# Kernel tuning notes

Measured on AMD Instinct MI355X. Metric: run time of the kernel, lower is better.

## Reference

```python
import jax, jax.numpy as jnp
import numpy as np

N = 100000   # nodes
E = 1600000  # edges
B = 64       # graphs
IN_CH = 6
HID = 64
EPS_BN = 1e-5


def _sage_conv(x, src, dst, Wl, bl, Wr, n_nodes):
    # PyG SAGEConv (mean aggr): out = lin_l(mean_{j in N(i)} x_j) + lin_r(x_i)
    msg = x[src]  # [E, F] gather
    s = jax.ops.segment_sum(msg, dst, num_segments=n_nodes)
    cnt = jax.ops.segment_sum(jnp.ones((msg.shape[0], 1), x.dtype), dst, num_segments=n_nodes)
    agg = s / jnp.maximum(cnt, 1.0)  # isolated nodes -> 0 (PyG scatter-mean behavior)
    return agg @ Wl + bl + x @ Wr


def _bn_relu(h, g, b):
    # BatchNorm1d over node dim (training stats, biased var), then ReLU
    mu = jnp.mean(h, axis=0)
    var = jnp.mean((h - mu) ** 2, axis=0)
    return jax.nn.relu((h - mu) * jax.lax.rsqrt(var + EPS_BN) * g + b)


def setup_inputs() -> dict:
    key = jax.random.key(0)
    ks = jax.random.split(key, 20)
    def w(k, shape, fan_in):
        return jax.random.normal(k, shape, jnp.float32) * (1.0 / np.sqrt(fan_in))
    inp = {
        'x': jax.random.normal(ks[0], (N, IN_CH), jnp.float32),
        'edge_index': jax.random.randint(ks[1], (2, E), 0, N, jnp.int64),
        'batch': jnp.sort(jax.random.randint(ks[2], (N,), 0, B, jnp.int64)),
        'W1l': w(ks[3], (IN_CH, HID), IN_CH), 'b1': jnp.zeros((HID,), jnp.float32), 'W1r': w(ks[4], (IN_CH, HID), IN_CH),
        'W2l': w(ks[5], (HID, HID), HID), 'b2': jnp.zeros((HID,), jnp.float32), 'W2r': w(ks[6], (HID, HID), HID),
        'W3l': w(ks[7], (HID, HID), HID), 'b3': jnp.zeros((HID,), jnp.float32), 'W3r': w(ks[8], (HID, HID), HID),
        'g1': jnp.ones((HID,), jnp.float32), 'be1': jnp.zeros((HID,), jnp.float32),
        'g2': jnp.ones((HID,), jnp.float32), 'be2': jnp.zeros((HID,), jnp.float32),
        'g3': jnp.ones((HID,), jnp.float32), 'be3': jnp.zeros((HID,), jnp.float32),
        'phW1': w(ks[9], (HID, 32), HID), 'phb1': jnp.zeros((32,), jnp.float32),
        'phW2': w(ks[10], (32, 3), 32), 'phb2': jnp.zeros((3,), jnp.float32),
        'trW1': w(ks[11], (HID, 16), HID), 'trb1': jnp.zeros((16,), jnp.float32),
        'trW2': w(ks[12], (16, 1), 16), 'trb2': jnp.zeros((1,), jnp.float32),
    }
    return inp


def reference(x, edge_index, batch, W1l, b1, W1r, W2l, b2, W2r, W3l, b3, W3r,
              g1, be1, g2, be2, g3, be3, phW1, phb1, phW2, phb2, trW1, trb1, trW2, trb2):
    src, dst = edge_index[0], edge_index[1]
    n = x.shape[0]
    h = _bn_relu(_sage_conv(x, src, dst, W1l, b1, W1r, n), g1, be1)
    h = _bn_relu(_sage_conv(h, src, dst, W2l, b2, W2r, n), g2, be2)
    h = _bn_relu(_sage_conv(h, src, dst, W3l, b3, W3r, n), g3, be3)
    # persistence-weighted attention: softmax over ALL nodes (dim=0), as in the original
    pw = x[:, 4]
    pw = pw - jnp.min(pw)
    attn = jax.nn.softmax(pw + 1e-8, axis=0)  # [N]
    h_att = h * attn[:, None]
    # global mean pool per graph
    s = jax.ops.segment_sum(h_att, batch, num_segments=B)
    cnt = jax.ops.segment_sum(jnp.ones((n, 1), h.dtype), batch, num_segments=B)
    pool = s / jnp.maximum(cnt, 1.0)
    phase_logits = jax.nn.relu(pool @ phW1 + phb1) @ phW2 + phb2
    transition_prob = jax.nn.sigmoid(jax.nn.relu(pool @ trW1 + trb1) @ trW2 + trb2)
    return (phase_logits, transition_prob)
```

## Files before the change

kernel.cpp:

```cpp
#include <hip/hip_runtime.h>
#include <hip/hip_fp16.h>
#include <cstdint>
#include <cstddef>


#define EPB 8192
#define NBIN 512
#define EPS_BN 1e-5f

typedef _Float16 f16x8 __attribute__((ext_vector_type(8)));
typedef float    f32x4 __attribute__((ext_vector_type(4)));
typedef float    f32x2 __attribute__((ext_vector_type(2)));

__global__ __launch_bounds__(256) void bucket_hist(const int* __restrict__ dst,
                                                   int* __restrict__ blockBin,
                                                   int* __restrict__ binTotal, int E)
{
    __shared__ int hist[NBIN];
    int t = threadIdx.x;
    for (int i = t; i < NBIN; i += 256) hist[i] = 0;
    __syncthreads();
    int e0 = blockIdx.x * EPB;
#pragma unroll
    for (int k = 0; k < 32; k++) {
        int e = e0 + (k << 8) + t;
        if (e < E) atomicAdd(&hist[dst[e] >> 8], 1);
    }
    __syncthreads();
    for (int i = t; i < NBIN; i += 256) {
        int c = hist[i];
        blockBin[blockIdx.x * NBIN + i] = c;
        if (c) atomicAdd(&binTotal[i], c);
    }
}

__global__ __launch_bounds__(512) void bin_scan_totals(const int* __restrict__ binTotal,
                                                       int* __restrict__ binBase,
                                                       int* __restrict__ rowptrN)
{
    __shared__ int s[NBIN];
    int t = threadIdx.x;
    int tot = binTotal[t];
    s[t] = tot;
    __syncthreads();
    for (int off = 1; off < NBIN; off <<= 1) {
        int v = (t >= off) ? s[t - off] : 0;
        __syncthreads();
        s[t] += v;
        __syncthreads();
    }
    binBase[t] = s[t] - tot;
    if (t == NBIN - 1) { binBase[NBIN] = s[t]; *rowptrN = s[t]; }
}

__global__ __launch_bounds__(256) void blockbin_offs(int* __restrict__ blockBin,
                                                     const int* __restrict__ binBase,
                                                     int nBlk)
{
    int wv   = threadIdx.x >> 6;
    int lane = threadIdx.x & 63;
    int bin  = blockIdx.x * 4 + wv;
    int carry = binBase[bin];
    for (int c0 = 0; c0 < nBlk; c0 += 64) {
        int blk = c0 + lane;
        int cnt = (blk < nBlk) ? blockBin[blk * NBIN + bin] : 0;
        int v = cnt;
#pragma unroll
        for (int d = 1; d < 64; d <<= 1) {
            int u = __shfl_up(v, d, 64);
            if (lane >= d) v += u;
        }
        if (blk < nBlk) blockBin[blk * NBIN + bin] = carry + v - cnt;
        carry += __shfl(v, 63, 64);
    }
}

__global__ __launch_bounds__(256) void bucket_scatter(const int* __restrict__ src,
                                                      const int* __restrict__ dst,
                                                      const int* __restrict__ blockBin,
                                                      int* __restrict__ epck, int E)
{
    __shared__ int cur[NBIN];
    int t = threadIdx.x;
    for (int i = t; i < NBIN; i += 256) cur[i] = blockBin[blockIdx.x * NBIN + i];
    __syncthreads();
    int e0 = blockIdx.x * EPB;
#pragma unroll
    for (int k = 0; k < 32; k++) {
        int e = e0 + (k << 8) + t;
        if (e < E) {
            int d = dst[e];
            int pos = atomicAdd(&cur[d >> 8], 1);
            epck[pos] = src[e] | ((d & 255) << 24);
        }
    }
}

__global__ __launch_bounds__(256) void csr_local(const int* __restrict__ epck,
                                                 const int* __restrict__ binBase,
                                                 int* __restrict__ rowptr,
                                                 int* __restrict__ eidx, int N)
{
    __shared__ int cnt[256], s[256], cur[256];
    int t = threadIdx.x, bkt = blockIdx.x;
    int base = binBase[bkt], nE = binBase[bkt + 1] - base;
    cnt[t] = 0;
    __syncthreads();
    for (int j = t; j < nE; j += 256)
        atomicAdd(&cnt[(unsigned)epck[base + j] >> 24], 1);
    __syncthreads();
    s[t] = cnt[t];
    __syncthreads();
    for (int off = 1; off < 256; off <<= 1) {
        int v = (t >= off) ? s[t - off] : 0;
        __syncthreads();
        s[t] += v;
        __syncthreads();
    }
    int excl = s[t] - cnt[t];
    cur[t] = excl;
    int node = (bkt << 8) + t;
    if (node < N) rowptr[node] = base + excl;
    __syncthreads();
    for (int j = t; j < nE; j += 256) {
        int v = epck[base + j];
        int pos = atomicAdd(&cur[(unsigned)v >> 24], 1);
        eidx[base + pos] = v & 0xFFFFFF;
    }
}

__global__ __launch_bounds__(256) void w_prep(const float* __restrict__ Wl,
                                              const float* __restrict__ Wr,
                                              __half* __restrict__ wf)
{
    int i = blockIdx.x * 256 + threadIdx.x;
    if (i >= 8192) return;
    int j    = i & 7;
    int m    = (i >> 3) & 15;
    int quad = (i >> 7) & 3;
    int tt   = (i >> 9) & 3;
    int q    = i >> 11;
    int k    = (q & 1) * 32 + quad * 8 + j;
    int col  = tt * 16 + m;
    const float* W = (q < 2) ? Wl : Wr;
    wf[i] = __float2half_rn(W[k * 64 + col]);
}

__global__ __launch_bounds__(256) void sage1_fused(
    const int* __restrict__ rowptr, const int* __restrict__ eidx,
    const float* __restrict__ x,
    const float* __restrict__ Wl, const float* __restrict__ bias,
    const float* __restrict__ Wr, float* __restrict__ out, int n)
{
    __shared__ float4 sWl[6 * 16];
    __shared__ float4 sWr[6 * 16];
    for (int i = threadIdx.x; i < 6 * 16; i += 256) {
        sWl[i] = ((const float4*)Wl)[i];
        sWr[i] = ((const float4*)Wr)[i];
    }
    __syncthreads();

    int node = blockIdx.x * 256 + threadIdx.x;
    if (node >= n) return;

    int b = rowptr[node], e = rowptr[node + 1];
    float a[6] = {0.f, 0.f, 0.f, 0.f, 0.f, 0.f};
    for (int j = b; j < e; j++) {
        int s = eidx[j];
        const float2* r = (const float2*)(x + (size_t)s * 6);
        float2 r0 = r[0], r1 = r[1], r2 = r[2];
        a[0] += r0.x; a[1] += r0.y; a[2] += r1.x;
        a[3] += r1.y; a[4] += r2.x; a[5] += r2.y;
    }
    float invd = 1.0f / fmaxf((float)(e - b), 1.0f);

    const float2* xr2 = (const float2*)(x + (size_t)node * 6);
    float2 x0 = xr2[0], x1 = xr2[1], x2 = xr2[2];
    float hh[6] = {x0.x, x0.y, x1.x, x1.y, x2.x, x2.y};

    float4 acc[16];
#pragma unroll
    for (int cg = 0; cg < 16; cg++) acc[cg] = ((const float4*)bias)[cg];
#pragma unroll
    for (int k = 0; k < 6; k++) {
        float am = a[k] * invd;
        float hk = hh[k];
#pragma unroll
        for (int cg = 0; cg < 16; cg++) {
            float4 wl = sWl[k * 16 + cg];
            float4 wr = sWr[k * 16 + cg];
            acc[cg].x = fmaf(am, wl.x, fmaf(hk, wr.x, acc[cg].x));
            acc[cg].y = fmaf(am, wl.y, fmaf(hk, wr.y, acc[cg].y));
            acc[cg].z = fmaf(am, wl.z, fmaf(hk, wr.z, acc[cg].z));
            acc[cg].w = fmaf(am, wl.w, fmaf(hk, wr.w, acc[cg].w));
        }
    }
    float4* orow = (float4*)(out + (size_t)node * 64);
#pragma unroll
    for (int cg = 0; cg < 16; cg++) orow[cg] = acc[cg];
}

__global__ __launch_bounds__(256) void bn_stats(const float* __restrict__ h,
                                                float* __restrict__ stats, size_t total)
{
    __shared__ float ls[64], lss[64];
    if (threadIdx.x < 64) { ls[threadIdx.x] = 0.f; lss[threadIdx.x] = 0.f; }
    __syncthreads();
    float s = 0.f, ss = 0.f;
    size_t stride = (size_t)gridDim.x * 256;
    for (size_t i = (size_t)blockIdx.x * 256 + threadIdx.x; i < total; i += stride) {
        float v = h[i];
        s += v;
        ss = fmaf(v, v, ss);
    }
    int c = threadIdx.x & 63;
    atomicAdd(&ls[c], s);
    atomicAdd(&lss[c], ss);
    __syncthreads();
    if (threadIdx.x < 64) {
        unsafeAtomicAdd(&stats[threadIdx.x], ls[threadIdx.x]);
        unsafeAtomicAdd(&stats[64 + threadIdx.x], lss[threadIdx.x]);
    }
}

__global__ __launch_bounds__(128) void stats_reduce(const float* __restrict__ tmp,
                                                    float* __restrict__ stats)
{
    int t = threadIdx.x;
    float s = 0.f;
#pragma unroll 8
    for (int k = 0; k < 64; k++) s += tmp[k * 128 + t];
    stats[t] = s;
}

__global__ __launch_bounds__(256) void bn_dual(const float* __restrict__ h,
                                               const float* __restrict__ stats,
                                               const float* __restrict__ g,
                                               const float* __restrict__ be,
                                               __half* __restrict__ h16,
                                               unsigned* __restrict__ h8,
                                               float invN, size_t total)
{
    size_t i4 = (size_t)blockIdx.x * 256 + threadIdx.x;
    if (i4 * 4 >= total) return;
    int c0 = (int)((i4 * 4) & 63);
    float v[4];
    float4 hv = ((const float4*)h)[i4];
    float hh[4] = {hv.x, hv.y, hv.z, hv.w};
#pragma unroll
    for (int j = 0; j < 4; j++) {
        int c = c0 + j;
        float mu  = stats[c] * invN;
        float var = stats[64 + c] * invN - mu * mu;
        float sc  = g[c] / sqrtf(var + EPS_BN);
        float sh  = fmaf(-mu, sc, be[c]);
        v[j] = fmaxf(fmaf(hh[j], sc, sh), 0.f);
    }
    float2 o16;
    ((__half2*)&o16)[0] = __floats2half2_rn(v[0], v[1]);
    ((__half2*)&o16)[1] = __floats2half2_rn(v[2], v[3]);
    ((float2*)h16)[i4] = o16;
    int p = __builtin_amdgcn_cvt_pk_fp8_f32(v[0], v[1], 0, false);
    p     = __builtin_amdgcn_cvt_pk_fp8_f32(v[2], v[3], p, true);
    h8[i4] = (unsigned)p;
}

__global__ __launch_bounds__(256) void aggpull8(const int* __restrict__ rowptr,
                                                const int* __restrict__ eidx,
                                                const unsigned* __restrict__ h8,
                                                __half* __restrict__ agg16, int n)
{
    int wid  = (blockIdx.x * 256 + threadIdx.x) >> 6;
    int lane = threadIdx.x & 63;
    int grp  = lane >> 4;
    int cq   = lane & 15;
    int node = wid * 4 + grp;
    if (node >= n) return;
    int b = rowptr[node], e = rowptr[node + 1];

    float4 a0 = {0,0,0,0}, a1 = {0,0,0,0}, a2 = {0,0,0,0}, a3 = {0,0,0,0};

#define EDGE(S, ACC)                                                            \
    {                                                                           \
        unsigned r_ = h8[(size_t)(S) * 16 + cq];                                \
        f32x2 lo_ = __builtin_amdgcn_cvt_pk_f32_fp8(r_, false);                 \
        f32x2 hi_ = __builtin_amdgcn_cvt_pk_f32_fp8(r_, true);                  \
        ACC.x += lo_[0]; ACC.y += lo_[1]; ACC.z += hi_[0]; ACC.w += hi_[1];     \
    }

    int j = b;
    for (; j + 4 <= e; j += 4) {
        int s0 = eidx[j], s1 = eidx[j + 1], s2 = eidx[j + 2], s3 = eidx[j + 3];
        EDGE(s0, a0) EDGE(s1, a1) EDGE(s2, a2) EDGE(s3, a3)
    }
    for (; j < e; j++) {
        int s = eidx[j];
        EDGE(s, a0)
    }
#undef EDGE

    float ax = a0.x + a1.x + a2.x + a3.x;
    float ay = a0.y + a1.y + a2.y + a3.y;
    float az = a0.z + a1.z + a2.z + a3.z;
    float aw = a0.w + a1.w + a2.w + a3.w;
    float invd = 1.0f / fmaxf((float)(e - b), 1.0f);
    __half2 o01 = __floats2half2_rn(ax * invd, ay * invd);
    __half2 o23 = __floats2half2_rn(az * invd, aw * invd);
    float2 ov;
    ((__half2*)&ov)[0] = o01;
    ((__half2*)&ov)[1] = o23;
    ((float2*)(agg16 + (size_t)node * 64))[cq] = ov;
}

__global__ __launch_bounds__(256) void mm_mfma(
    const __half* __restrict__ agg16, const __half* __restrict__ h16,
    const __half* __restrict__ wfh, const float* __restrict__ bias,
    float* __restrict__ out, float* __restrict__ statsTmp, int n)
{
    __shared__ float ls[64], lss[64];
    int t = threadIdx.x;
    if (t < 64) { ls[t] = 0.f; lss[t] = 0.f; }
    __syncthreads();

    int wv = t >> 6, lane = t & 63;
    int m = lane & 15, quad = lane >> 4;
    int node0 = (blockIdx.x * 4 + wv) * 16;

    if (node0 < n) {
        const f16x8* wf = (const f16x8*)wfh;

        int nodeA = node0 + m;
        if (nodeA >= n) nodeA = n - 1;

        const _Float16* arow = (const _Float16*)(agg16 + (size_t)nodeA * 64);
        const _Float16* hrow = (const _Float16*)(h16   + (size_t)nodeA * 64);
        f16x8 af[4];
        af[0] = *(const f16x8*)(arow + quad * 8);
        af[1] = *(const f16x8*)(arow + 32 + quad * 8);
        af[2] = *(const f16x8*)(hrow + quad * 8);
        af[3] = *(const f16x8*)(hrow + 32 + quad * 8);

#pragma unroll
        for (int tt = 0; tt < 4; tt++) {
            float bv = bias[tt * 16 + m];
            f32x4 c = {bv, bv, bv, bv};
#pragma unroll
            for (int q = 0; q < 4; q++)
                c = __builtin_amdgcn_mfma_f32_16x16x32_f16(
                        af[q], wf[((q * 4 + tt) * 4 + quad) * 16 + m], c, 0, 0, 0);
            float s = 0.f, ss = 0.f;
#pragma unroll
            for (int r = 0; r < 4; r++) {
                int row = node0 + quad * 4 + r;
                float v = (row < n) ? c[r] : 0.f;
                if (row < n) out[(size_t)row * 64 + tt * 16 + m] = v;
                s += v;
                ss = fmaf(v, v, ss);
            }
            s  += __shfl_xor(s, 16, 64);  s  += __shfl_xor(s, 32, 64);
            ss += __shfl_xor(ss, 16, 64); ss += __shfl_xor(ss, 32, 64);
            if (quad == 0) {
                atomicAdd(&ls[tt * 16 + m], s);
                atomicAdd(&lss[tt * 16 + m], ss);
            }
        }
    }
    __syncthreads();
    if (t < 64) {
        float* slot = statsTmp + (size_t)(blockIdx.x & 63) * 128;
        unsafeAtomicAdd(&slot[t], ls[t]);
        unsafeAtomicAdd(&slot[64 + t], lss[t]);
    }
}

__global__ __launch_bounds__(256) void bn_pool(
    const float* __restrict__ h, const float* __restrict__ stats,
    const float* __restrict__ g, const float* __restrict__ be,
    const float* __restrict__ x, const int* __restrict__ batch,
    float* __restrict__ rawpool, float invN, int N, int chunk)
{
    int wid  = blockIdx.x * 4 + (threadIdx.x >> 6);
    int lane = threadIdx.x & 63;
    int i0 = wid * chunk;
    if (i0 >= N) return;
    int i1 = min(i0 + chunk, N);

    float mu  = stats[lane] * invN;
    float var = stats[64 + lane] * invN - mu * mu;
    float sc  = g[lane] / sqrtf(var + EPS_BN);
    float sh  = fmaf(-mu, sc, be[lane]);

    int   cur = batch[i0];
    float acc = 0.f;
    for (int i = i0; i < i1; i++) {
        int bi = batch[i];
        if (bi != cur) {
            unsafeAtomicAdd(&rawpool[cur * 64 + lane], acc);
            acc = 0.f;
            cur = bi;
        }
        float w = expf(x[(size_t)i * 6 + 4]);
        float v = fmaxf(fmaf(h[(size_t)i * 64 + lane], sc, sh), 0.f);
        acc = fmaf(v, w, acc);
    }
    unsafeAtomicAdd(&rawpool[cur * 64 + lane], acc);
}

__global__ __launch_bounds__(256) void softmax_sum(const float* __restrict__ x,
                                                   float* __restrict__ sumexp, int n)
{
    float s = 0.f;
    int stride = gridDim.x * 256;
    for (int i = blockIdx.x * 256 + threadIdx.x; i < n; i += stride)
        s += expf(x[(size_t)i * 6 + 4]);
#pragma unroll
    for (int o = 32; o > 0; o >>= 1) s += __shfl_down(s, o, 64);
    __shared__ float wsum[4];
    if ((threadIdx.x & 63) == 0) wsum[threadIdx.x >> 6] = s;
    __syncthreads();
    if (threadIdx.x == 0)
        unsafeAtomicAdd(sumexp, wsum[0] + wsum[1] + wsum[2] + wsum[3]);
}

__global__ void seg_bounds(const int* __restrict__ batch, int* __restrict__ lb, int n)
{
    int b = threadIdx.x;
    if (b > 64) return;
    int lo = 0, hi = n;
    while (lo < hi) {
        int mid = (lo + hi) >> 1;
        if (batch[mid] < b) lo = mid + 1; else hi = mid;
    }
    lb[b] = lo;
}

__global__ __launch_bounds__(64) void heads_kernel(
    const float* __restrict__ rawpool, const float* __restrict__ sumexp,
    const int* __restrict__ lb,
    const float* __restrict__ phW1, const float* __restrict__ phb1,
    const float* __restrict__ phW2, const float* __restrict__ phb2,
    const float* __restrict__ trW1, const float* __restrict__ trb1,
    const float* __restrict__ trW2, const float* __restrict__ trb2,
    float* __restrict__ out)
{
    int b = blockIdx.x, t = threadIdx.x;
    __shared__ float p[64], h1[32], h2[16];
    float cnt = (float)(lb[b + 1] - lb[b]);
    p[t] = rawpool[b * 64 + t] / (sumexp[0] * fmaxf(cnt, 1.0f));
    __syncthreads();
    if (t < 32) {
        float s = phb1[t];
        for (int k = 0; k < 64; k++) s = fmaf(p[k], phW1[k * 32 + t], s);
        h1[t] = fmaxf(s, 0.f);
    } else if (t < 48) {
        int tt = t - 32;
        float s = trb1[tt];
        for (int k = 0; k < 64; k++) s = fmaf(p[k], trW1[k * 16 + tt], s);
        h2[tt] = fmaxf(s, 0.f);
    }
    __syncthreads();
    if (t < 3) {
        float s = phb2[t];
        for (int k = 0; k < 32; k++) s = fmaf(h1[k], phW2[k * 3 + t], s);
        out[b * 3 + t] = s;
    } else if (t == 63) {
        float s = trb2[0];
        for (int k = 0; k < 16; k++) s = fmaf(h2[k], trW2[k], s);
        out[192 + b] = 1.0f / (1.0f + expf(-s));
    }
}

extern "C" void kernel_launch(void* const* d_in, const int* in_sizes, int n_in,
                              void* d_out, int out_size, void* d_ws, size_t ws_size,
                              hipStream_t stream)
{
    const float* x     = (const float*)d_in[0];
    const int*   ei    = (const int*)d_in[1];
    const int*   batch = (const int*)d_in[2];
    const float* W1l = (const float*)d_in[3];
    const float* b1  = (const float*)d_in[4];
    const float* W1r = (const float*)d_in[5];
    const float* W2l = (const float*)d_in[6];
    const float* b2  = (const float*)d_in[7];
    const float* W2r = (const float*)d_in[8];
    const float* W3l = (const float*)d_in[9];
    const float* b3  = (const float*)d_in[10];
    const float* W3r = (const float*)d_in[11];
    const float* g1  = (const float*)d_in[12];
    const float* be1 = (const float*)d_in[13];
    const float* g2  = (const float*)d_in[14];
    const float* be2 = (const float*)d_in[15];
    const float* g3  = (const float*)d_in[16];
    const float* be3 = (const float*)d_in[17];
    const float* phW1 = (const float*)d_in[18];
    const float* phb1 = (const float*)d_in[19];
    const float* phW2 = (const float*)d_in[20];
    const float* phb2 = (const float*)d_in[21];
    const float* trW1 = (const float*)d_in[22];
    const float* trb1 = (const float*)d_in[23];
    const float* trW2 = (const float*)d_in[24];
    const float* trb2 = (const float*)d_in[25];

    const int N = in_sizes[0] / 6;
    const int E = in_sizes[1] / 2;
    const int* src = ei;
    const int* dst = ei + E;

    const int NB    = (N + 255) >> 8;
    const int nBlkA = (E + EPB - 1) / EPB;

    float* ws = (float*)d_ws;
    const size_t N64 = (size_t)N * 64;
    float*  hA      = ws;
    float*  hB      = ws + N64;
    __half* agg16   = (__half*)(ws + 2 * N64);
    __half* h16     = (__half*)(ws + 2 * N64 + N64 / 2);
    int*   epck     = (int*)(ws + 3 * N64);
    int*   eidx     = epck + E;
    int*   blockBin = eidx + E;
    int*   binTotal = blockBin + (size_t)nBlkA * NBIN;
    float* stats    = (float*)(binTotal + NBIN);
    float* statsTmp = stats + 384;
    float* rawpool  = statsTmp + 16384;
    float* sumexp   = rawpool + 4096;
    int*   binBase  = (int*)(sumexp + 4);
    int*   rowptr   = binBase + NBIN + 1;
    int*   lb       = rowptr + N + 1;
    __half* wfrag2  = (__half*)(lb + 72);
    __half* wfrag3  = wfrag2 + 8192;
    unsigned* h8    = (unsigned*)(wfrag3 + 8192);
    float* out      = (float*)d_out;

    const int nodeBlocks = (N + 255) / 256;
    const int aggBlocks  = (N + 15) / 16;
    const int mfmaBlocks = (N + 63) / 64;
    const int cvt4Blocks = (int)((N64 / 4 + 255) / 256);
    const int PBLK = 1024;
    const int chunk = (N + PBLK * 4 - 1) / (PBLK * 4);
    const float invN = 1.0f / (float)N;

    size_t zbytes = (char*)(sumexp + 4) - (char*)binTotal;
    hipMemsetAsync(binTotal, 0, zbytes, stream);
    softmax_sum<<<256, 256, 0, stream>>>(x, sumexp, N);
    seg_bounds<<<1, 128, 0, stream>>>(batch, lb, N);
    w_prep<<<32, 256, 0, stream>>>(W2l, W2r, wfrag2);
    w_prep<<<32, 256, 0, stream>>>(W3l, W3r, wfrag3);

    bucket_hist<<<nBlkA, 256, 0, stream>>>(dst, blockBin, binTotal, E);
    bin_scan_totals<<<1, NBIN, 0, stream>>>(binTotal, binBase, rowptr + N);
    blockbin_offs<<<NBIN / 4, 256, 0, stream>>>(blockBin, binBase, nBlkA);
    bucket_scatter<<<nBlkA, 256, 0, stream>>>(src, dst, blockBin, epck, E);
    csr_local<<<NB, 256, 0, stream>>>(epck, binBase, rowptr, eidx, N);

    sage1_fused<<<nodeBlocks, 256, 0, stream>>>(rowptr, eidx, x, W1l, b1, W1r, hA, N);
    bn_stats<<<1024, 256, 0, stream>>>(hA, stats, N64);
    bn_dual<<<cvt4Blocks, 256, 0, stream>>>(hA, stats, g1, be1, h16, h8, invN, N64);

    aggpull8<<<aggBlocks, 256, 0, stream>>>(rowptr, eidx, h8, agg16, N);
    mm_mfma<<<mfmaBlocks, 256, 0, stream>>>(agg16, h16, wfrag2, b2, hB,
                                            statsTmp, N);
    stats_reduce<<<1, 128, 0, stream>>>(statsTmp, stats + 128);
    bn_dual<<<cvt4Blocks, 256, 0, stream>>>(hB, stats + 128, g2, be2, h16, h8,
                                            invN, N64);

    aggpull8<<<aggBlocks, 256, 0, stream>>>(rowptr, eidx, h8, agg16, N);
    mm_mfma<<<mfmaBlocks, 256, 0, stream>>>(agg16, h16, wfrag3, b3, hA,
                                            statsTmp + 8192, N);
    stats_reduce<<<1, 128, 0, stream>>>(statsTmp + 8192, stats + 256);

    bn_pool<<<PBLK, 256, 0, stream>>>(hA, stats + 256, g3, be3, x, batch,
                                      rawpool, invN, N, chunk);
    heads_kernel<<<64, 64, 0, stream>>>(rawpool, sumexp, lb,
                                        phW1, phb1, phW2, phb2,
                                        trW1, trb1, trW2, trb2, out);
}
```

Measured before the change: 381.0 us.

## Fuse CSR local build with first SAGE layer aggregation and transform

```diff
diff --git a/kernel.cpp b/kernel.cpp
--- a/kernel.cpp
+++ b/kernel.cpp
@@ -96,37 +96,83 @@
     }
 }
 
-__global__ __launch_bounds__(256) void csr_local(const int* __restrict__ epck,
-                                                 const int* __restrict__ binBase,
-                                                 int* __restrict__ rowptr,
-                                                 int* __restrict__ eidx, int N)
-{
-    __shared__ int cnt[256], s[256], cur[256];
+__global__ __launch_bounds__(256) void csr_sage1(
+    const int* __restrict__ epck, const int* __restrict__ binBase,
+    const float* __restrict__ x,
+    const float* __restrict__ Wl, const float* __restrict__ bias,
+    const float* __restrict__ Wr,
+    int* __restrict__ rowptr, int* __restrict__ eidx,
+    float* __restrict__ out, int N)
+{
+    __shared__ int    cnt[256], scn[256], cur[256];
+    __shared__ float  a6[256 * 6];
+    __shared__ float4 sWl[96], sWr[96];
     int t = threadIdx.x, bkt = blockIdx.x;
     int base = binBase[bkt], nE = binBase[bkt + 1] - base;
     cnt[t] = 0;
+    if (t < 96) { sWl[t] = ((const float4*)Wl)[t]; sWr[t] = ((const float4*)Wr)[t]; }
+    for (int i = t; i < 1536; i += 256) a6[i] = 0.f;
     __syncthreads();
     for (int j = t; j < nE; j += 256)
         atomicAdd(&cnt[(unsigned)epck[base + j] >> 24], 1);
     __syncthreads();
-    s[t] = cnt[t];
+    scn[t] = cnt[t];
     __syncthreads();
     for (int off = 1; off < 256; off <<= 1) {
-        int v = (t >= off) ? s[t - off] : 0;
+        int v = (t >= off) ? scn[t - off] : 0;
         __syncthreads();
-        s[t] += v;
+        scn[t] += v;
         __syncthreads();
     }
-    int excl = s[t] - cnt[t];
+    int excl = scn[t] - cnt[t];
     cur[t] = excl;
     int node = (bkt << 8) + t;
     if (node < N) rowptr[node] = base + excl;
     __syncthreads();
     for (int j = t; j < nE; j += 256) {
-        int v = epck[base + j];
-        int pos = atomicAdd(&cur[(unsigned)v >> 24], 1);
-        eidx[base + pos] = v & 0xFFFFFF;
-    }
+        int v  = epck[base + j];
+        int dl = (unsigned)v >> 24;
+        int s_ = v & 0xFFFFFF;
+        int pos = atomicAdd(&cur[dl], 1);
+        eidx[base + pos] = s_;
+        const float2* r = (const float2*)(x + (size_t)s_ * 6);
+        float2 r0 = r[0], r1 = r[1], r2 = r[2];
+        atomicAdd(&a6[dl * 6 + 0], r0.x); atomicAdd(&a6[dl * 6 + 1], r0.y);
+        atomicAdd(&a6[dl * 6 + 2], r1.x); atomicAdd(&a6[dl * 6 + 3], r1.y);
+        atomicAdd(&a6[dl * 6 + 4], r2.x); atomicAdd(&a6[dl * 6 + 5], r2.y);
+    }
+    __syncthreads();
+    if (node >= N) return;
+
+    float invd = 1.0f / fmaxf((float)cnt[t], 1.0f);
+    float a[6];
+#pragma unroll
+    for (int k = 0; k < 6; k++) a[k] = a6[t * 6 + k] * invd;
+
+    const float2* xr2 = (const float2*)(x + (size_t)node * 6);
+    float2 x0 = xr2[0], x1 = xr2[1], x2 = xr2[2];
+    float hh[6] = {x0.x, x0.y, x1.x, x1.y, x2.x, x2.y};
+
+    float4 acc[16];
+#pragma unroll
+    for (int cg = 0; cg < 16; cg++) acc[cg] = ((const float4*)bias)[cg];
+#pragma unroll
+    for (int k = 0; k < 6; k++) {
+        float am = a[k];
+        float hk = hh[k];
+#pragma unroll
+        for (int cg = 0; cg < 16; cg++) {
+            float4 wl = sWl[k * 16 + cg];
+            float4 wr = sWr[k * 16 + cg];
+            acc[cg].x = fmaf(am, wl.x, fmaf(hk, wr.x, acc[cg].x));
+            acc[cg].y = fmaf(am, wl.y, fmaf(hk, wr.y, acc[cg].y));
+            acc[cg].z = fmaf(am, wl.z, fmaf(hk, wr.z, acc[cg].z));
+            acc[cg].w = fmaf(am, wl.w, fmaf(hk, wr.w, acc[cg].w));
+        }
+    }
+    float4* orow = (float4*)(out + (size_t)node * 64);
+#pragma unroll
+    for (int cg = 0; cg < 16; cg++) orow[cg] = acc[cg];
 }
 
 __global__ __launch_bounds__(256) void w_prep(const float* __restrict__ Wl,
@@ -144,60 +190,6 @@
     int col  = tt * 16 + m;
     const float* W = (q < 2) ? Wl : Wr;
     wf[i] = __float2half_rn(W[k * 64 + col]);
-}
-
-__global__ __launch_bounds__(256) void sage1_fused(
-    const int* __restrict__ rowptr, const int* __restrict__ eidx,
-    const float* __restrict__ x,
-    const float* __restrict__ Wl, const float* __restrict__ bias,
-    const float* __restrict__ Wr, float* __restrict__ out, int n)
-{
-    __shared__ float4 sWl[6 * 16];
-    __shared__ float4 sWr[6 * 16];
-    for (int i = threadIdx.x; i < 6 * 16; i += 256) {
-        sWl[i] = ((const float4*)Wl)[i];
-        sWr[i] = ((const float4*)Wr)[i];
-    }
-    __syncthreads();
-
-    int node = blockIdx.x * 256 + threadIdx.x;
-    if (node >= n) return;
-
-    int b = rowptr[node], e = rowptr[node + 1];
-    float a[6] = {0.f, 0.f, 0.f, 0.f, 0.f, 0.f};
-    for (int j = b; j < e; j++) {
-        int s = eidx[j];
-        const float2* r = (const float2*)(x + (size_t)s * 6);
-        float2 r0 = r[0], r1 = r[1], r2 = r[2];
-        a[0] += r0.x; a[1] += r0.y; a[2] += r1.x;
-        a[3] += r1.y; a[4] += r2.x; a[5] += r2.y;
-    }
-    float invd = 1.0f / fmaxf((float)(e - b), 1.0f);
-
-    const float2* xr2 = (const float2*)(x + (size_t)node * 6);
-    float2 x0 = xr2[0], x1 = xr2[1], x2 = xr2[2];
-    float hh[6] = {x0.x, x0.y, x1.x, x1.y, x2.x, x2.y};
-
-    float4 acc[16];
-#pragma unroll
-    for (int cg = 0; cg < 16; cg++) acc[cg] = ((const float4*)bias)[cg];
-#pragma unroll
-    for (int k = 0; k < 6; k++) {
-        float am = a[k] * invd;
-        float hk = hh[k];
-#pragma unroll
-        for (int cg = 0; cg < 16; cg++) {
-            float4 wl = sWl[k * 16 + cg];
-            float4 wr = sWr[k * 16 + cg];
-            acc[cg].x = fmaf(am, wl.x, fmaf(hk, wr.x, acc[cg].x));
-            acc[cg].y = fmaf(am, wl.y, fmaf(hk, wr.y, acc[cg].y));
-            acc[cg].z = fmaf(am, wl.z, fmaf(hk, wr.z, acc[cg].z));
-            acc[cg].w = fmaf(am, wl.w, fmaf(hk, wr.w, acc[cg].w));
-        }
-    }
-    float4* orow = (float4*)(out + (size_t)node * 64);
-#pragma unroll
-    for (int cg = 0; cg < 16; cg++) orow[cg] = acc[cg];
 }
 
 __global__ __launch_bounds__(256) void bn_stats(const float* __restrict__ h,
@@ -531,7 +523,6 @@
     unsigned* h8    = (unsigned*)(wfrag3 + 8192);
     float* out      = (float*)d_out;
 
-    const int nodeBlocks = (N + 255) / 256;
     const int aggBlocks  = (N + 15) / 16;
     const int mfmaBlocks = (N + 63) / 64;
     const int cvt4Blocks = (int)((N64 / 4 + 255) / 256);
@@ -550,9 +541,9 @@
     bin_scan_totals<<<1, NBIN, 0, stream>>>(binTotal, binBase, rowptr + N);
     blockbin_offs<<<NBIN / 4, 256, 0, stream>>>(blockBin, binBase, nBlkA);
     bucket_scatter<<<nBlkA, 256, 0, stream>>>(src, dst, blockBin, epck, E);
-    csr_local<<<NB, 256, 0, stream>>>(epck, binBase, rowptr, eidx, N);
-
-    sage1_fused<<<nodeBlocks, 256, 0, stream>>>(rowptr, eidx, x, W1l, b1, W1r, hA, N);
+    csr_sage1<<<NB, 256, 0, stream>>>(epck, binBase, x, W1l, b1, W1r,
+                                      rowptr, eidx, hA, N);
+
     bn_stats<<<1024, 256, 0, stream>>>(hA, stats, N64);
     bn_dual<<<cvt4Blocks, 256, 0, stream>>>(hA, stats, g1, be1, h16, h8, invN, N64);
 
```

New measurement: 419.6 us. 10.1% more time.

## Fuse neighbor aggregation into MFMA matmul kernel via shared-memory tile

Applied to the files above, without the earlier changes.

```diff
diff --git a/kernel.cpp b/kernel.cpp
--- a/kernel.cpp
+++ b/kernel.cpp
@@ -265,78 +265,71 @@
     h8[i4] = (unsigned)p;
 }
 
-__global__ __launch_bounds__(256) void aggpull8(const int* __restrict__ rowptr,
-                                                const int* __restrict__ eidx,
-                                                const unsigned* __restrict__ h8,
-                                                __half* __restrict__ agg16, int n)
-{
-    int wid  = (blockIdx.x * 256 + threadIdx.x) >> 6;
-    int lane = threadIdx.x & 63;
-    int grp  = lane >> 4;
-    int cq   = lane & 15;
-    int node = wid * 4 + grp;
-    if (node >= n) return;
-    int b = rowptr[node], e = rowptr[node + 1];
-
-    float4 a0 = {0,0,0,0}, a1 = {0,0,0,0}, a2 = {0,0,0,0}, a3 = {0,0,0,0};
-
-#define EDGE(S, ACC)                                                            \
-    {                                                                           \
-        unsigned r_ = h8[(size_t)(S) * 16 + cq];                                \
-        f32x2 lo_ = __builtin_amdgcn_cvt_pk_f32_fp8(r_, false);                 \
-        f32x2 hi_ = __builtin_amdgcn_cvt_pk_f32_fp8(r_, true);                  \
-        ACC.x += lo_[0]; ACC.y += lo_[1]; ACC.z += hi_[0]; ACC.w += hi_[1];     \
-    }
-
-    int j = b;
-    for (; j + 4 <= e; j += 4) {
-        int s0 = eidx[j], s1 = eidx[j + 1], s2 = eidx[j + 2], s3 = eidx[j + 3];
-        EDGE(s0, a0) EDGE(s1, a1) EDGE(s2, a2) EDGE(s3, a3)
-    }
-    for (; j < e; j++) {
-        int s = eidx[j];
-        EDGE(s, a0)
-    }
-#undef EDGE
-
-    float ax = a0.x + a1.x + a2.x + a3.x;
-    float ay = a0.y + a1.y + a2.y + a3.y;
-    float az = a0.z + a1.z + a2.z + a3.z;
-    float aw = a0.w + a1.w + a2.w + a3.w;
-    float invd = 1.0f / fmaxf((float)(e - b), 1.0f);
-    __half2 o01 = __floats2half2_rn(ax * invd, ay * invd);
-    __half2 o23 = __floats2half2_rn(az * invd, aw * invd);
-    float2 ov;
-    ((__half2*)&ov)[0] = o01;
-    ((__half2*)&ov)[1] = o23;
-    ((float2*)(agg16 + (size_t)node * 64))[cq] = ov;
-}
-
-__global__ __launch_bounds__(256) void mm_mfma(
-    const __half* __restrict__ agg16, const __half* __restrict__ h16,
+#define TSTRIDE 72
+__global__ __launch_bounds__(256) void agg_mm_mfma(
+    const int* __restrict__ rowptr, const int* __restrict__ eidx,
+    const unsigned* __restrict__ h8, const __half* __restrict__ h16,
     const __half* __restrict__ wfh, const float* __restrict__ bias,
     float* __restrict__ out, float* __restrict__ statsTmp, int n)
 {
     __shared__ float ls[64], lss[64];
+    __shared__ _Float16 sT[4][16 * TSTRIDE];
     int t = threadIdx.x;
     if (t < 64) { ls[t] = 0.f; lss[t] = 0.f; }
-    __syncthreads();
 
     int wv = t >> 6, lane = t & 63;
+    int node0 = (blockIdx.x * 4 + wv) * 16;
+
+    int grp = lane >> 4, cq = lane & 15;
+#pragma unroll 1
+    for (int r = 0; r < 4; r++) {
+        int node = node0 + r * 4 + grp;
+        int b = 0, e = 0;
+        if (node < n) { b = rowptr[node]; e = rowptr[node + 1]; }
+
+        float4 a0 = {0,0,0,0}, a1 = {0,0,0,0}, a2 = {0,0,0,0}, a3 = {0,0,0,0};
+#define EDGE(S, ACC)                                                            \
+        {                                                                       \
+            unsigned r_ = h8[(size_t)(S) * 16 + cq];                            \
+            f32x2 lo_ = __builtin_amdgcn_cvt_pk_f32_fp8(r_, false);             \
+            f32x2 hi_ = __builtin_amdgcn_cvt_pk_f32_fp8(r_, true);              \
+            ACC.x += lo_[0]; ACC.y += lo_[1]; ACC.z += hi_[0]; ACC.w += hi_[1]; \
+        }
+        int j = b;
+        for (; j + 4 <= e; j += 4) {
+            int s0 = eidx[j], s1 = eidx[j + 1], s2 = eidx[j + 2], s3 = eidx[j + 3];
+            EDGE(s0, a0) EDGE(s1, a1) EDGE(s2, a2) EDGE(s3, a3)
+        }
+        for (; j < e; j++) {
+            int s = eidx[j];
+            EDGE(s, a0)
+        }
+#undef EDGE
+        float ax = a0.x + a1.x + a2.x + a3.x;
+        float ay = a0.y + a1.y + a2.y + a3.y;
+        float az = a0.z + a1.z + a2.z + a3.z;
+        float aw = a0.w + a1.w + a2.w + a3.w;
+        float invd = 1.0f / fmaxf((float)(e - b), 1.0f);
+        __half2 o01 = __floats2half2_rn(ax * invd, ay * invd);
+        __half2 o23 = __floats2half2_rn(az * invd, aw * invd);
+        float2 ov;
+        ((__half2*)&ov)[0] = o01;
+        ((__half2*)&ov)[1] = o23;
+        *(float2*)(&sT[wv][(r * 4 + grp) * TSTRIDE + cq * 4]) = ov;
+    }
+    __syncthreads();
+
     int m = lane & 15, quad = lane >> 4;
-    int node0 = (blockIdx.x * 4 + wv) * 16;
-
     if (node0 < n) {
         const f16x8* wf = (const f16x8*)wfh;
 
         int nodeA = node0 + m;
         if (nodeA >= n) nodeA = n - 1;
 
-        const _Float16* arow = (const _Float16*)(agg16 + (size_t)nodeA * 64);
-        const _Float16* hrow = (const _Float16*)(h16   + (size_t)nodeA * 64);
+        const _Float16* hrow = (const _Float16*)(h16 + (size_t)nodeA * 64);
         f16x8 af[4];
-        af[0] = *(const f16x8*)(arow + quad * 8);
-        af[1] = *(const f16x8*)(arow + 32 + quad * 8);
+        af[0] = *(const f16x8*)(&sT[wv][m * TSTRIDE + quad * 8]);
+        af[1] = *(const f16x8*)(&sT[wv][m * TSTRIDE + 32 + quad * 8]);
         af[2] = *(const f16x8*)(hrow + quad * 8);
         af[3] = *(const f16x8*)(hrow + 32 + quad * 8);
 
@@ -530,9 +523,9 @@
     __half* wfrag3  = wfrag2 + 8192;
     unsigned* h8    = (unsigned*)(wfrag3 + 8192);
     float* out      = (float*)d_out;
+    (void)agg16;
 
     const int nodeBlocks = (N + 255) / 256;
-    const int aggBlocks  = (N + 15) / 16;
     const int mfmaBlocks = (N + 63) / 64;
     const int cvt4Blocks = (int)((N64 / 4 + 255) / 256);
     const int PBLK = 1024;
@@ -556,16 +549,14 @@
     bn_stats<<<1024, 256, 0, stream>>>(hA, stats, N64);
     bn_dual<<<cvt4Blocks, 256, 0, stream>>>(hA, stats, g1, be1, h16, h8, invN, N64);
 
-    aggpull8<<<aggBlocks, 256, 0, stream>>>(rowptr, eidx, h8, agg16, N);
-    mm_mfma<<<mfmaBlocks, 256, 0, stream>>>(agg16, h16, wfrag2, b2, hB,
-                                            statsTmp, N);
+    agg_mm_mfma<<<mfmaBlocks, 256, 0, stream>>>(rowptr, eidx, h8, h16, wfrag2, b2,
+                                                hB, statsTmp, N);
     stats_reduce<<<1, 128, 0, stream>>>(statsTmp, stats + 128);
     bn_dual<<<cvt4Blocks, 256, 0, stream>>>(hB, stats + 128, g2, be2, h16, h8,
                                             invN, N64);
 
-    aggpull8<<<aggBlocks, 256, 0, stream>>>(rowptr, eidx, h8, agg16, N);
-    mm_mfma<<<mfmaBlocks, 256, 0, stream>>>(agg16, h16, wfrag3, b3, hA,
-                                            statsTmp + 8192, N);
+    agg_mm_mfma<<<mfmaBlocks, 256, 0, stream>>>(rowptr, eidx, h8, h16, wfrag3, b3,
+                                                hA, statsTmp + 8192, N);
     stats_reduce<<<1, 128, 0, stream>>>(statsTmp + 8192, stats + 256);
 
     bn_pool<<<PBLK, 256, 0, stream>>>(hA, stats + 256, g3, be3, x, batch,
```

Measured after the change: 372.8 us. -2.1%, faster.
